# Kernel optimization log

Hardware: AMD Instinct MI355X
Metric: run time of the kernel (lower is better)

## Reference

```python
import jax, jax.numpy as jnp
import numpy as np

ODIM = 8192      # output dim (slice target)
MSIZE = 64       # tile size
N_BLOCKS = 1024  # size of shared block bank


def setup_inputs() -> dict:
    key = jax.random.key(0)
    k1, k2, k3, k4 = jax.random.split(key, 4)
    x = jax.random.normal(k1, (256, 8192), dtype=jnp.float32)
    # bank of msize x msize module blocks (scaled like fan-in init)
    blocks = jax.random.normal(k2, (N_BLOCKS, MSIZE, MSIZE), dtype=jnp.float32) * 0.02
    bound = 1.0 / np.sqrt(ODIM).astype(np.float32)
    bias = jax.random.uniform(k3, (ODIM,), dtype=jnp.float32, minval=-bound, maxval=bound)
    # parts: [icount, ocount] indices into the block bank
    parts = jax.random.randint(k4, (128, 128), 0, N_BLOCKS)
    return {"x": x, "blocks": blocks, "bias": bias, "parts": parts}


def reference(x, blocks, bias, parts):
    icount, ocount = parts.shape
    m = blocks.shape[-1]
    # build_mosaic: gather blocks per parts and tile into a dense weight matrix
    fc = blocks[parts]                                   # [ic, oc, m, m]
    fc_mat = fc.transpose(0, 2, 1, 3).reshape(icount * m, ocount * m)
    # idim (8192) is divisible by msize, so pad is identity (rem == 0 branch)
    y = x @ fc_mat                                       # [B, oc*m]
    y = y[..., :ODIM] + bias                             # slice + bias; post = Identity
    return y
```

## Files before the change

kernel.cpp:

```cpp
#include <hip/hip_runtime.h>
#include <stdint.h>

#define BATCH 256
#define IDIM  8192
#define ODIM  8192
#define MS    64
#define IC    128
#define OC    128
#define NB    1024

#define TM 64
#define TN 128
#define KSPLIT 2
#define IB_PER (IC / KSPLIT)

typedef __bf16 bf16x8 __attribute__((ext_vector_type(8)));
typedef float  floatx4 __attribute__((ext_vector_type(4)));

__device__ __forceinline__ void async_load16(unsigned short* lds_p, const unsigned short* g_p) {
    __builtin_amdgcn_global_load_lds(
        (const __attribute__((address_space(1))) unsigned int*)g_p,
        (__attribute__((address_space(3))) unsigned int*)lds_p,
        16, 0, 0);
}

__device__ __forceinline__ unsigned short f32_to_bf16(float f) {
    unsigned int u = __float_as_uint(f);
    u += 0x7FFFu + ((u >> 16) & 1u);
    return (unsigned short)(u >> 16);
}

__global__ void k_convert_x(const float* __restrict__ x, unsigned short* __restrict__ xb) {
    int t = blockIdx.x * 256 + threadIdx.x;
    const float4* x4 = (const float4*)x;
    float4 a = x4[2 * t], b = x4[2 * t + 1];
    union { unsigned short s[8]; uint4 v; } u;
    u.s[0] = f32_to_bf16(a.x); u.s[1] = f32_to_bf16(a.y);
    u.s[2] = f32_to_bf16(a.z); u.s[3] = f32_to_bf16(a.w);
    u.s[4] = f32_to_bf16(b.x); u.s[5] = f32_to_bf16(b.y);
    u.s[6] = f32_to_bf16(b.z); u.s[7] = f32_to_bf16(b.w);
    ((uint4*)xb)[t] = u.v;
}

__global__ void k_convert_blocks(const float* __restrict__ blocks, unsigned short* __restrict__ bt) {
    __shared__ float tile[MS][MS + 1];
    int b = blockIdx.x;
    const float4* src4 = (const float4*)(blocks + (size_t)b * MS * MS);
    unsigned short* dst = bt + (size_t)b * MS * MS;
    #pragma unroll
    for (int i = 0; i < 4; ++i) {
        int slot = i * 256 + threadIdx.x;
        int r = slot >> 4, c4 = (slot & 15) * 4;
        float4 v = src4[slot];
        tile[r][c4 + 0] = v.x; tile[r][c4 + 1] = v.y;
        tile[r][c4 + 2] = v.z; tile[r][c4 + 3] = v.w;
    }
    __syncthreads();
    #pragma unroll
    for (int i = 0; i < 2; ++i) {
        int slot = i * 256 + threadIdx.x;
        int c = slot >> 3, o = slot & 7;
        union { unsigned short s[8]; uint4 v; } u;
        #pragma unroll
        for (int j = 0; j < 8; ++j) u.s[j] = f32_to_bf16(tile[o * 8 + j][c]);
        *(uint4*)(dst + c * MS + o * 8) = u.v;
    }
}

__global__ __launch_bounds__(256, 2)
void k_mosaic_gemm(const unsigned short* __restrict__ xb,
                   const unsigned short* __restrict__ bt,
                   const int* __restrict__ parts,
                   float* __restrict__ partial) {
    __shared__ __align__(16) unsigned short a_lds[TM * MS];
    __shared__ __align__(16) unsigned short b_lds[TN * MS];

    const int tid  = threadIdx.x;
    const int lane = tid & 63;
    const int wave = tid >> 6;
    const int nt = blockIdx.x;
    const int mt = blockIdx.y;
    const int ks = blockIdx.z;

    const int m0  = mt * TM;
    const int ob0 = nt * (TN / MS);
    const int ib0 = ks * IB_PER;

    const int row  = lane & 15;
    const int quad = lane >> 4;

    int a_off[2][4], b_off[2][2];
    #pragma unroll
    for (int kk = 0; kk < 2; ++kk) {
        int oct = kk * 4 + quad;
        #pragma unroll
        for (int mi = 0; mi < 4; ++mi) {
            int r = mi * 16 + row;
            a_off[kk][mi] = r * MS + ((oct ^ (r & 7)) << 3);
        }
        #pragma unroll
        for (int ni = 0; ni < 2; ++ni) {
            int n = wave * 32 + ni * 16 + row;
            b_off[kk][ni] = n * MS + ((oct ^ (n & 7)) << 3);
        }
    }

    floatx4 acc[4][2];
    #pragma unroll
    for (int mi = 0; mi < 4; ++mi)
        #pragma unroll
        for (int ni = 0; ni < 2; ++ni)
            acc[mi][ni] = (floatx4){0.f, 0.f, 0.f, 0.f};

    for (int ib = ib0; ib < ib0 + IB_PER; ++ib) {
        int p0 = parts[ib * OC + ob0];
        int p1 = parts[ib * OC + ob0 + 1];

        #pragma unroll
        for (int j = 0; j < 2; ++j) {
            int slot = j * 256 + tid;
            int m = slot >> 3;
            int oct = (slot & 7) ^ (m & 7);
            async_load16(&a_lds[slot * 8],
                         xb + (size_t)(m0 + m) * IDIM + ib * MS + oct * 8);
        }
        #pragma unroll
        for (int j = 0; j < 4; ++j) {
            int slot = j * 256 + tid;
            int n = slot >> 3;
            int oct = (slot & 7) ^ (n & 7);
            int p = (j < 2) ? p0 : p1;
            async_load16(&b_lds[slot * 8],
                         bt + (size_t)p * (MS * MS) + (n & 63) * MS + oct * 8);
        }
        __syncthreads();

        #pragma unroll
        for (int kk = 0; kk < 2; ++kk) {
            bf16x8 af[4], bfr[2];
            #pragma unroll
            for (int mi = 0; mi < 4; ++mi)
                af[mi] = *(const bf16x8*)&a_lds[a_off[kk][mi]];
            #pragma unroll
            for (int ni = 0; ni < 2; ++ni)
                bfr[ni] = *(const bf16x8*)&b_lds[b_off[kk][ni]];
            #pragma unroll
            for (int mi = 0; mi < 4; ++mi)
                #pragma unroll
                for (int ni = 0; ni < 2; ++ni)
                    acc[mi][ni] = __builtin_amdgcn_mfma_f32_16x16x32_bf16(
                        af[mi], bfr[ni], acc[mi][ni], 0, 0, 0);
        }
        __syncthreads();
    }

    float* out = partial + (size_t)ks * BATCH * ODIM;
    const int cbase = nt * TN + wave * 32;
    #pragma unroll
    for (int mi = 0; mi < 4; ++mi)
        #pragma unroll
        for (int ni = 0; ni < 2; ++ni)
            #pragma unroll
            for (int r = 0; r < 4; ++r) {
                int rowg = m0 + mi * 16 + quad * 4 + r;
                int colg = cbase + ni * 16 + row;
                out[(size_t)rowg * ODIM + colg] = acc[mi][ni][r];
            }
}

__global__ void k_reduce_bias(const float* __restrict__ partial,
                              const float* __restrict__ bias,
                              float* __restrict__ out) {
    int t = blockIdx.x * 256 + threadIdx.x;
    const float4* p0 = (const float4*)partial;
    const float4* p1 = (const float4*)(partial + (size_t)BATCH * ODIM);
    const float4* b4 = (const float4*)bias;
    float4 a = p0[t], b = p1[t], c = b4[t & (ODIM / 4 - 1)];
    float4 r;
    r.x = a.x + b.x + c.x; r.y = a.y + b.y + c.y;
    r.z = a.z + b.z + c.z; r.w = a.w + b.w + c.w;
    ((float4*)out)[t] = r;
}

extern "C" void kernel_launch(void* const* d_in, const int* in_sizes, int n_in,
                              void* d_out, int out_size, void* d_ws, size_t ws_size,
                              hipStream_t stream) {
    const float* x      = (const float*)d_in[0];
    const float* blocks = (const float*)d_in[1];
    const float* bias   = (const float*)d_in[2];
    const int*   parts  = (const int*)d_in[3];
    float* out = (float*)d_out;

    char* ws = (char*)d_ws;
    unsigned short* xb      = (unsigned short*)ws;
    unsigned short* btively = (unsigned short*)(ws + (4u << 20));
    float*          partial = (float*)(ws + (12u << 20));

    k_convert_x<<<(BATCH * IDIM) / (256 * 8), 256, 0, stream>>>(x, xb);
    k_convert_blocks<<<NB, 256, 0, stream>>>(blocks, btively);
    k_mosaic_gemm<<<dim3(ODIM / TN, BATCH / TM, KSPLIT), 256, 0, stream>>>(xb, btively, parts, partial);
    k_reduce_bias<<<(BATCH * ODIM) / (256 * 4), 256, 0, stream>>>(partial, bias, out);
}
```

Measured before the change: 142.6 us.

## Enlarge GEMM tile to 128x128 with 2x2 wave layout, split-K 4, fuse convert kernels

Doubles the M tile to 128 and arranges the four waves in a 2x2 grid, so each wave computes a 64x64 sub-tile and operand fragments loaded from LDS are reused more. Split-K rises from 2 to 4 to keep the grid at 512 blocks, and the reduction kernel now sums four partial buffers. The two bf16 conversion kernels are merged into one launch. In exchange, the larger accumulators raise register pressure, and the extra partial buffers add global memory traffic in the reduction.

```diff
diff --git a/kernel.cpp b/kernel.cpp
--- a/kernel.cpp
+++ b/kernel.cpp
@@ -9,9 +9,9 @@
 #define OC    128
 #define NB    1024
 
-#define TM 64
+#define TM 128
 #define TN 128
-#define KSPLIT 2
+#define KSPLIT 4
 #define IB_PER (IC / KSPLIT)
 
 typedef __bf16 bf16x8 __attribute__((ext_vector_type(8)));
@@ -30,40 +30,41 @@
     return (unsigned short)(u >> 16);
 }
 
-__global__ void k_convert_x(const float* __restrict__ x, unsigned short* __restrict__ xb) {
-    int t = blockIdx.x * 256 + threadIdx.x;
-    const float4* x4 = (const float4*)x;
-    float4 a = x4[2 * t], b = x4[2 * t + 1];
-    union { unsigned short s[8]; uint4 v; } u;
-    u.s[0] = f32_to_bf16(a.x); u.s[1] = f32_to_bf16(a.y);
-    u.s[2] = f32_to_bf16(a.z); u.s[3] = f32_to_bf16(a.w);
-    u.s[4] = f32_to_bf16(b.x); u.s[5] = f32_to_bf16(b.y);
-    u.s[6] = f32_to_bf16(b.z); u.s[7] = f32_to_bf16(b.w);
-    ((uint4*)xb)[t] = u.v;
-}
-
-__global__ void k_convert_blocks(const float* __restrict__ blocks, unsigned short* __restrict__ bt) {
+__global__ void k_convert(const float* __restrict__ x, const float* __restrict__ blocks,
+                          unsigned short* __restrict__ xb, unsigned short* __restrict__ bt) {
     __shared__ float tile[MS][MS + 1];
     int b = blockIdx.x;
-    const float4* src4 = (const float4*)(blocks + (size_t)b * MS * MS);
-    unsigned short* dst = bt + (size_t)b * MS * MS;
-    #pragma unroll
-    for (int i = 0; i < 4; ++i) {
-        int slot = i * 256 + threadIdx.x;
-        int r = slot >> 4, c4 = (slot & 15) * 4;
-        float4 v = src4[slot];
-        tile[r][c4 + 0] = v.x; tile[r][c4 + 1] = v.y;
-        tile[r][c4 + 2] = v.z; tile[r][c4 + 3] = v.w;
-    }
-    __syncthreads();
-    #pragma unroll
-    for (int i = 0; i < 2; ++i) {
-        int slot = i * 256 + threadIdx.x;
-        int c = slot >> 3, o = slot & 7;
+    if (b < NB) {
+        const float4* src4 = (const float4*)(blocks + (size_t)b * MS * MS);
+        unsigned short* dst = bt + (size_t)b * MS * MS;
+        #pragma unroll
+        for (int i = 0; i < 4; ++i) {
+            int slot = i * 256 + threadIdx.x;
+            int r = slot >> 4, c4 = (slot & 15) * 4;
+            float4 v = src4[slot];
+            tile[r][c4 + 0] = v.x; tile[r][c4 + 1] = v.y;
+            tile[r][c4 + 2] = v.z; tile[r][c4 + 3] = v.w;
+        }
+        __syncthreads();
+        #pragma unroll
+        for (int i = 0; i < 2; ++i) {
+            int slot = i * 256 + threadIdx.x;
+            int c = slot >> 3, o = slot & 7;
+            union { unsigned short s[8]; uint4 v; } u;
+            #pragma unroll
+            for (int j = 0; j < 8; ++j) u.s[j] = f32_to_bf16(tile[o * 8 + j][c]);
+            *(uint4*)(dst + c * MS + o * 8) = u.v;
+        }
+    } else {
+        int t = (b - NB) * 256 + threadIdx.x;
+        const float4* x4 = (const float4*)x;
+        float4 a = x4[2 * t], bb = x4[2 * t + 1];
         union { unsigned short s[8]; uint4 v; } u;
-        #pragma unroll
-        for (int j = 0; j < 8; ++j) u.s[j] = f32_to_bf16(tile[o * 8 + j][c]);
-        *(uint4*)(dst + c * MS + o * 8) = u.v;
+        u.s[0] = f32_to_bf16(a.x);  u.s[1] = f32_to_bf16(a.y);
+        u.s[2] = f32_to_bf16(a.z);  u.s[3] = f32_to_bf16(a.w);
+        u.s[4] = f32_to_bf16(bb.x); u.s[5] = f32_to_bf16(bb.y);
+        u.s[6] = f32_to_bf16(bb.z); u.s[7] = f32_to_bf16(bb.w);
+        ((uint4*)xb)[t] = u.v;
     }
 }
 
@@ -78,6 +79,8 @@
     const int tid  = threadIdx.x;
     const int lane = tid & 63;
     const int wave = tid >> 6;
+    const int wrow = wave >> 1;
+    const int wcol = wave & 1;
     const int nt = blockIdx.x;
     const int mt = blockIdx.y;
     const int ks = blockIdx.z;
@@ -89,27 +92,27 @@
     const int row  = lane & 15;
     const int quad = lane >> 4;
 
-    int a_off[2][4], b_off[2][2];
+    int a_off[2][4], b_off[2][4];
     #pragma unroll
     for (int kk = 0; kk < 2; ++kk) {
         int oct = kk * 4 + quad;
         #pragma unroll
         for (int mi = 0; mi < 4; ++mi) {
-            int r = mi * 16 + row;
+            int r = wrow * 64 + mi * 16 + row;
             a_off[kk][mi] = r * MS + ((oct ^ (r & 7)) << 3);
         }
         #pragma unroll
-        for (int ni = 0; ni < 2; ++ni) {
-            int n = wave * 32 + ni * 16 + row;
+        for (int ni = 0; ni < 4; ++ni) {
+            int n = wcol * 64 + ni * 16 + row;
             b_off[kk][ni] = n * MS + ((oct ^ (n & 7)) << 3);
         }
     }
 
-    floatx4 acc[4][2];
+    floatx4 acc[4][4];
     #pragma unroll
     for (int mi = 0; mi < 4; ++mi)
         #pragma unroll
-        for (int ni = 0; ni < 2; ++ni)
+        for (int ni = 0; ni < 4; ++ni)
             acc[mi][ni] = (floatx4){0.f, 0.f, 0.f, 0.f};
 
     for (int ib = ib0; ib < ib0 + IB_PER; ++ib) {
@@ -117,7 +120,7 @@
         int p1 = parts[ib * OC + ob0 + 1];
 
         #pragma unroll
-        for (int j = 0; j < 2; ++j) {
+        for (int j = 0; j < 4; ++j) {
             int slot = j * 256 + tid;
             int m = slot >> 3;
             int oct = (slot & 7) ^ (m & 7);
@@ -137,17 +140,17 @@
 
         #pragma unroll
         for (int kk = 0; kk < 2; ++kk) {
-            bf16x8 af[4], bfr[2];
+            bf16x8 af[4], bfr[4];
             #pragma unroll
             for (int mi = 0; mi < 4; ++mi)
                 af[mi] = *(const bf16x8*)&a_lds[a_off[kk][mi]];
             #pragma unroll
-            for (int ni = 0; ni < 2; ++ni)
+            for (int ni = 0; ni < 4; ++ni)
                 bfr[ni] = *(const bf16x8*)&b_lds[b_off[kk][ni]];
             #pragma unroll
             for (int mi = 0; mi < 4; ++mi)
                 #pragma unroll
-                for (int ni = 0; ni < 2; ++ni)
+                for (int ni = 0; ni < 4; ++ni)
                     acc[mi][ni] = __builtin_amdgcn_mfma_f32_16x16x32_bf16(
                         af[mi], bfr[ni], acc[mi][ni], 0, 0, 0);
         }
@@ -155,15 +158,14 @@
     }
 
     float* out = partial + (size_t)ks * BATCH * ODIM;
-    const int cbase = nt * TN + wave * 32;
     #pragma unroll
     for (int mi = 0; mi < 4; ++mi)
         #pragma unroll
-        for (int ni = 0; ni < 2; ++ni)
+        for (int ni = 0; ni < 4; ++ni)
             #pragma unroll
             for (int r = 0; r < 4; ++r) {
-                int rowg = m0 + mi * 16 + quad * 4 + r;
-                int colg = cbase + ni * 16 + row;
+                int rowg = m0 + wrow * 64 + mi * 16 + quad * 4 + r;
+                int colg = nt * TN + wcol * 64 + ni * 16 + row;
                 out[(size_t)rowg * ODIM + colg] = acc[mi][ni][r];
             }
 }
@@ -172,13 +174,15 @@
                               const float* __restrict__ bias,
                               float* __restrict__ out) {
     int t = blockIdx.x * 256 + threadIdx.x;
-    const float4* p0 = (const float4*)partial;
-    const float4* p1 = (const float4*)(partial + (size_t)BATCH * ODIM);
     const float4* b4 = (const float4*)bias;
-    float4 a = p0[t], b = p1[t], c = b4[t & (ODIM / 4 - 1)];
-    float4 r;
-    r.x = a.x + b.x + c.x; r.y = a.y + b.y + c.y;
-    r.z = a.z + b.z + c.z; r.w = a.w + b.w + c.w;
+    float4 c = b4[t & (ODIM / 4 - 1)];
+    float4 r = {c.x, c.y, c.z, c.w};
+    #pragma unroll
+    for (int k = 0; k < KSPLIT; ++k) {
+        const float4* p = (const float4*)(partial + (size_t)k * BATCH * ODIM);
+        float4 a = p[t];
+        r.x += a.x; r.y += a.y; r.z += a.z; r.w += a.w;
+    }
     ((float4*)out)[t] = r;
 }
 
@@ -193,11 +197,10 @@
 
     char* ws = (char*)d_ws;
     unsigned short* xb      = (unsigned short*)ws;
-    unsigned short* btively = (unsigned short*)(ws + (4u << 20));
+    unsigned short* btb     = (unsigned short*)(ws + (4u << 20));
     float*          partial = (float*)(ws + (12u << 20));
 
-    k_convert_x<<<(BATCH * IDIM) / (256 * 8), 256, 0, stream>>>(x, xb);
-    k_convert_blocks<<<NB, 256, 0, stream>>>(blocks, btively);
-    k_mosaic_gemm<<<dim3(ODIM / TN, BATCH / TM, KSPLIT), 256, 0, stream>>>(xb, btively, parts, partial);
+    k_convert<<<NB + (BATCH * IDIM) / (256 * 8), 256, 0, stream>>>(x, blocks, xb, btb);
+    k_mosaic_gemm<<<dim3(ODIM / TN, BATCH / TM, KSPLIT), 256, 0, stream>>>(xb, btb, parts, partial);
     k_reduce_bias<<<(BATCH * ODIM) / (256 * 4), 256, 0, stream>>>(partial, bias, out);
 }
```

Result: faster. 125.5 us (-12.0%).
